# Performance work log

Hardware: AMD Instinct MI355X
Metric: run time of the kernel (lower is better)

Reference implementation:

```python
import jax, jax.numpy as jnp
import numpy as np

LAMBDA_SOFTMAX = 9.0  # opt.lambda_softmax (smooth)
LAMBDA_LSE = 6.0      # opt.lambda_lse (LogSumExp aggregation)
EPS = 1e-8


def l2norm(x, axis, eps=EPS):
    # matches torch l2norm: x / (sqrt(sum(x^2)) + eps)
    return x / (jnp.sqrt(jnp.sum(x * x, axis=axis, keepdims=True)) + eps)


def setup_inputs() -> dict:
    key = jax.random.key(0)
    k1, k2 = jax.random.split(key)
    images = jax.random.normal(k1, (128, 36, 256), dtype=jnp.float32)    # (n_image, n_regions, d)
    captions = jax.random.normal(k2, (256, 48, 256), dtype=jnp.float32)  # (n_caption, max_n_word, d)
    return {"images": images, "captions": captions}


def reference(images, captions):
    """Vectorized SCAN xattn_score_t2i with raw_feature_norm='clipped_l2norm',
    agg_func='LogSumExp'. Returns (n_image, n_caption) similarity matrix.
    Axes: c=caption, i=image, r=region (sourceL), w=word (queryL), d=embed."""
    # func_attention: attn = bmm(context, query^T) -> (b, sourceL, queryL); here batched over (c, i)
    attn = jnp.einsum('ird,cwd->cirw', images, captions)       # [c,i,r,w]
    # first norm: LeakyReLU(0.1) then l2norm over queryL dim (torch dim=2 of (b,r,w))
    attn = jax.nn.leaky_relu(attn, negative_slope=0.1)
    attn = l2norm(attn, axis=3)
    # transpose to (b, queryL, sourceL) and smoothed softmax over sourceL
    attn = jnp.swapaxes(attn, 2, 3)                            # [c,i,w,r]
    attn = jax.nn.softmax(attn * LAMBDA_SOFTMAX, axis=-1)
    # weightedContext = attn @ context  -> (b, queryL, d)
    wctx = jnp.einsum('ciwr,ird->ciwd', attn, images)          # [c,i,w,d]
    # cosine similarity over d between expanded caption words and weighted context
    cap = captions[:, None, :, :]                              # [c,1,w,d]
    w12 = jnp.sum(cap * wctx, axis=-1)                         # [c,i,w]
    w1 = jnp.sqrt(jnp.sum(cap * cap, axis=-1))
    w2 = jnp.sqrt(jnp.sum(wctx * wctx, axis=-1))
    row_sim = w12 / jnp.maximum(w1 * w2, EPS)                  # [c,i,w]
    # LogSumExp aggregation over words: log(sum exp(s*lse)) / lse
    sim = jax.scipy.special.logsumexp(row_sim * LAMBDA_LSE, axis=-1) / LAMBDA_LSE  # [c,i]
    return sim.T                                               # (n_image, n_caption)
```

## Files before the change

### kernel.cpp

```cpp
#include <hip/hip_runtime.h>
#include <math.h>

#define NI 128
#define NC 256
#define NR 36
#define NW 48
#define ND 256

#define PIB 264
#define PG  72
#define PSP 52

#define SOFT_SCALE 12.984255368000671f
#define LSE_SCALE   8.656170245333781f

typedef __bf16 bf16;
typedef __bf16 bf16x8 __attribute__((ext_vector_type(8)));
typedef __bf16 bf16x4 __attribute__((ext_vector_type(4)));
typedef float  f32x4  __attribute__((ext_vector_type(4)));

#define OFF_IB    0
#define OFF_G     19008
#define OFF_P     24192
#define OFF_GUARD 37504
#define SMEM_TOTAL 37632

#define MFMA16(A,B,C) __builtin_amdgcn_mfma_f32_16x16x32_bf16(A, B, C, 0, 0, 0)

__device__ __forceinline__ float dpp_add16(float v) {
    int x = __builtin_bit_cast(int, v);
    v += __builtin_bit_cast(float, __builtin_amdgcn_update_dpp(0, x, 0xB1, 0xF, 0xF, true));
    x = __builtin_bit_cast(int, v);
    v += __builtin_bit_cast(float, __builtin_amdgcn_update_dpp(0, x, 0x4E, 0xF, 0xF, true));
    x = __builtin_bit_cast(int, v);
    v += __builtin_bit_cast(float, __builtin_amdgcn_update_dpp(0, x, 0x141, 0xF, 0xF, true));
    x = __builtin_bit_cast(int, v);
    v += __builtin_bit_cast(float, __builtin_amdgcn_update_dpp(0, x, 0x140, 0xF, 0xF, true));
    return v;
}

__device__ __forceinline__ float lrelu(float t) {
    return __builtin_fmaf(0.55f, t, 0.45f * __builtin_fabsf(t));
}

__global__ __launch_bounds__(256)
void prep_kernel(const float* __restrict__ captions, bf16* __restrict__ capb,
                 float* __restrict__ w1g)
{
    const int c = blockIdx.x >> 2, q = blockIdx.x & 3;
    const int wave = threadIdx.x >> 6, lane = threadIdx.x & 63;
    #pragma unroll
    for (int j = 0; j < 3; ++j) {
        int w = q * 12 + wave * 3 + j;
        size_t off = ((size_t)c * NW + w) * ND + lane * 4;
        float4 v = *(const float4*)(captions + off);
        bf16x4 h = { (bf16)v.x, (bf16)v.y, (bf16)v.z, (bf16)v.w };
        *(bf16x4*)(capb + off) = h;
        float s = v.x*v.x + v.y*v.y + v.z*v.z + v.w*v.w;
        s += __shfl_xor(s, 1);  s += __shfl_xor(s, 2);  s += __shfl_xor(s, 4);
        s += __shfl_xor(s, 8);  s += __shfl_xor(s, 16); s += __shfl_xor(s, 32);
        if (lane == 0) w1g[c * NW + w] = LSE_SCALE / sqrtf(s);
    }
}

__device__ __forceinline__ bf16x8 ld_cvt_f32(const float* p, float& ss) {
    float4 lo = *(const float4*)p;
    float4 hi = *(const float4*)(p + 4);
    ss += lo.x*lo.x + lo.y*lo.y + lo.z*lo.z + lo.w*lo.w
        + hi.x*hi.x + hi.y*hi.y + hi.z*hi.z + hi.w*hi.w;
    bf16x8 r = { (bf16)lo.x, (bf16)lo.y, (bf16)lo.z, (bf16)lo.w,
                 (bf16)hi.x, (bf16)hi.y, (bf16)hi.z, (bf16)hi.w };
    return r;
}

#define STAGE_W(MT, BUF, W12) do {                                                      \
    _Pragma("unroll")                                                                   \
    for (int p = 0; p < 4; ++p) {                                                       \
        float a0v = acc[MT][0][p], a1v = acc[MT][1][p], a2v = acc[MT][2][p];            \
        float e0 = exp2f(__builtin_fmaf(c1[0], a0v, c2[0] * __builtin_fabsf(a0v)));     \
        float e1 = exp2f(__builtin_fmaf(c1[1], a1v, c2[1] * __builtin_fabsf(a1v)));     \
        float e2 = (l15 >= 12)                                                          \
            ? exp2f(__builtin_fmaf(c1[2], a2v, c2[2] * __builtin_fabsf(a2v)))           \
            : 0.f;                                                   \
        W12[p] = e0 * a0v + e1 * a1v + e2 * a2v;                                        \
        acc[MT][0][p] = e0; acc[MT][1][p] = e1; acc[MT][2][p] = e2;       \
        int row = quad * 4 + p;                                                         \
        (BUF)[row * PSP + l15]      = (bf16)e0;                                         \
        (BUF)[row * PSP + 16 + l15] = (bf16)e1;                                         \
        if (l15 >= 12) (BUF)[row * PSP + rb2 + l15] = (bf16)e2;        \
    }                                                                                   \
} while (0)

#define STAGE_R(MT, BUF, W12) do {                                                      \
    const bf16* ap = (BUF) + l15 * PSP;                                                 \
    bf16x8 pa0 = *(const bf16x8*)(ap + quad * 8);                                       \
    bf16x8 pa1 = *(const bf16x8*)(ap + 32 + quad * 8);  \
    f32x4 pg0 = {0,0,0,0}, pg1 = {0,0,0,0}, pg2 = {0,0,0,0};                            \
    {                                                                                   \
        bf16x8 t0 = *(const bf16x8*)&sG[(l15) * PG + quad * 8];                         \
        bf16x8 t1 = *(const bf16x8*)&sG[(l15) * PG + 32 + quad * 8];                    \
        pg0 = MFMA16(pa0, t0, pg0); pg0 = MFMA16(pa1, t1, pg0);                         \
        bf16x8 t2 = *(const bf16x8*)&sG[(16 + l15) * PG + quad * 8];                    \
        bf16x8 t3 = *(const bf16x8*)&sG[(16 + l15) * PG + 32 + quad * 8];               \
        pg1 = MFMA16(pa0, t2, pg1); pg1 = MFMA16(pa1, t3, pg1);                         \
        bf16x8 t4 = *(const bf16x8*)&sG[(rb2 + l15) * PG + quad * 8];                   \
        bf16x8 t5 = *(const bf16x8*)&sG[(rb2 + l15) * PG + 32 + quad * 8];              \
        pg2 = MFMA16(pa0, t4, pg2); pg2 = MFMA16(pa1, t5, pg2);                         \
    }                                                                                   \
    float4 wq = {0.f, 0.f, 0.f, 0.f};                                                   \
    if constexpr (USE_WS)                                                               \
        wq = *(const float4*)&w1g[(size_t)c * NW + (MT) * 16 + quad * 4];               \
    _Pragma("unroll")                                                                   \
    for (int p = 0; p < 4; ++p) {                                                       \
        float s2 = pg0[p] * acc[MT][0][p] + pg1[p] * acc[MT][1][p]                      \
                 + pg2[p] * acc[MT][2][p];                       \
        s2 = dpp_add16(s2);                                                             \
        float w12 = dpp_add16(W12[p]);                                                  \
        float wf = USE_WS ? ((const float*)&wq)[p] : w1f[MT][p];                        \
        esum += exp2f(w12 * __frsqrt_rn(fmaxf(s2, 1e-16f)) * wf);                       \
    }                                                                                   \
} while (0)

template<bool USE_WS>
__global__ __attribute__((amdgpu_flat_work_group_size(256, 256), amdgpu_waves_per_eu(4, 8)))
void scan_main(const float* __restrict__ images,
               const float* __restrict__ captions,
               const bf16* __restrict__ capb,
               const float* __restrict__ w1g,
               float* __restrict__ out)
{
    __shared__ __align__(16) unsigned char smem[SMEM_TOTAL];
    bf16* sIb = (bf16*)(smem + OFF_IB);
    bf16* sG  = (bf16*)(smem + OFF_G);

    const int tid  = threadIdx.x;
    const int wave = tid >> 6;
    const int lane = tid & 63;
    const int quad = lane >> 4;
    const int l15  = lane & 15;
    const int i    = blockIdx.x >> 4;
    const int c0   = (blockIdx.x & 15) * 16;

    bf16* bufA = (bf16*)(smem + OFF_P) + wave * (32 * PSP);
    bf16* bufB = bufA + 16 * PSP;

    const int rb2 = 20;

    const float* gI = images + (size_t)i * NR * ND;
    #pragma unroll
    for (int k = 0; k < 9; ++k) {
        int t = tid + k * 256;
        int e = t * 4, r = e >> 8, d = e & 255;
        float4 v = *(const float4*)(gI + e);
        bf16x4 h = { (bf16)v.x, (bf16)v.y, (bf16)v.z, (bf16)v.w };
        *(bf16x4*)&sIb[r * PIB + d] = h;
    }
    {
        uint32_t* pG = (uint32_t*)sG;
        #pragma unroll
        for (int k = 0; k < 6; ++k) { int x = tid + k * 256; if (x < 1296) pG[x] = 0u; }
        uint32_t* pP = (uint32_t*)(smem + OFF_P);
        #pragma unroll
        for (int k = 0; k < 14; ++k) { int x = tid + k * 256; if (x < 3360) pP[x] = 0u; }
    }
    __syncthreads();

    if (wave < 3) {
        const int mb = (wave == 2) ? rb2 : wave * 16;
        f32x4 g0 = {0,0,0,0}, g1 = {0,0,0,0}, g2 = {0,0,0,0};
        #pragma unroll
        for (int ks = 0; ks < 8; ++ks) {
            bf16x8 a  = *(const bf16x8*)&sIb[(mb + l15)  * PIB + ks * 32 + quad * 8];
            bf16x8 b0 = *(const bf16x8*)&sIb[(l15)       * PIB + ks * 32 + quad * 8];
            bf16x8 b1 = *(const bf16x8*)&sIb[(16 + l15)  * PIB + ks * 32 + quad * 8];
            bf16x8 b2 = *(const bf16x8*)&sIb[(rb2 + l15) * PIB + ks * 32 + quad * 8];
            g0 = MFMA16(a, b0, g0); g1 = MFMA16(a, b1, g1); g2 = MFMA16(a, b2, g2);
        }
        #pragma unroll
        for (int p = 0; p < 4; ++p) {
            int m = mb + quad * 4 + p;
            sG[m * PG + l15]       = (bf16)g0[p];
            sG[m * PG + 16 + l15]  = (bf16)g1[p];
            sG[m * PG + rb2 + l15] = (bf16)g2[p];
        }
    }
    __syncthreads();

    for (int it = 0; it < 4; ++it) {
        const int c = c0 + wave * 4 + it;

        f32x4 acc[3][3] = {};
        float ssc[3] = {0.f, 0.f, 0.f};
        float w1f[3][4] = {};
        const bf16*  ab   = USE_WS ? capb + ((size_t)c * NW + l15) * ND + quad * 8 : nullptr;
        const float* ab32 = USE_WS ? nullptr : captions + ((size_t)c * NW + l15) * ND + quad * 8;
        #pragma unroll
        for (int ks = 0; ks < 8; ++ks) {
            bf16x8 a0, a1, a2;
            if (USE_WS) {
                a0 = *(const bf16x8*)(ab + ks * 32);
                a1 = *(const bf16x8*)(ab + 16 * ND + ks * 32);
                a2 = *(const bf16x8*)(ab + 32 * ND + ks * 32);
            } else {
                a0 = ld_cvt_f32(ab32 + ks * 32, ssc[0]);
                a1 = ld_cvt_f32(ab32 + 16 * ND + ks * 32, ssc[1]);
                a2 = ld_cvt_f32(ab32 + 32 * ND + ks * 32, ssc[2]);
            }
            bf16x8 b0 = *(const bf16x8*)&sIb[(l15)       * PIB + ks * 32 + quad * 8];
            bf16x8 b1 = *(const bf16x8*)&sIb[(16 + l15)  * PIB + ks * 32 + quad * 8];
            bf16x8 b2 = *(const bf16x8*)&sIb[(rb2 + l15) * PIB + ks * 32 + quad * 8];
            acc[0][0] = MFMA16(a0, b0, acc[0][0]);
            acc[1][0] = MFMA16(a1, b0, acc[1][0]);
            acc[2][0] = MFMA16(a2, b0, acc[2][0]);
            acc[0][1] = MFMA16(a0, b1, acc[0][1]);
            acc[1][1] = MFMA16(a1, b1, acc[1][1]);
            acc[2][1] = MFMA16(a2, b1, acc[2][1]);
            acc[0][2] = MFMA16(a0, b2, acc[0][2]);
            acc[1][2] = MFMA16(a1, b2, acc[1][2]);
            acc[2][2] = MFMA16(a2, b2, acc[2][2]);
        }
        if (!USE_WS) {
            #pragma unroll
            for (int mt = 0; mt < 3; ++mt) {
                float s = ssc[mt];
                s += __shfl_xor(s, 16); s += __shfl_xor(s, 32);
                ssc[mt] = LSE_SCALE * __frsqrt_rn(fmaxf(s, 1e-16f));
            }
            #pragma unroll
            for (int mt = 0; mt < 3; ++mt)
                #pragma unroll
                for (int p = 0; p < 4; ++p)
                    w1f[mt][p] = __shfl(ssc[mt], (lane & 48) + quad * 4 + p);
        }

        float c1[3], c2[3];
        #pragma unroll
        for (int nt = 0; nt < 3; ++nt) {
            float s = 0.f;
            #pragma unroll
            for (int mt = 0; mt < 3; ++mt)
                #pragma unroll
                for (int p = 0; p < 4; ++p) { float t = lrelu(acc[mt][nt][p]); s += t * t; }
            s += __shfl_xor(s, 16); s += __shfl_xor(s, 32);
            float inv = SOFT_SCALE * __frsqrt_rn(fmaxf(s, 1e-12f));
            c1[nt] = 0.55f * inv;
            c2[nt] = 0.45f * inv;
        }

        float esum = 0.f;
        float w12a[4], w12b[4], w12c[4];
        STAGE_W(0, bufA, w12a);
        STAGE_W(1, bufB, w12b);
        STAGE_R(0, bufA, w12a);
        STAGE_W(2, bufA, w12c);
        STAGE_R(1, bufB, w12b);
        STAGE_R(2, bufA, w12c);

        esum += __shfl_xor(esum, 16); esum += __shfl_xor(esum, 32);
        if (lane == 0) out[(size_t)i * NC + c] = logf(esum) * (1.0f / 6.0f);
    }
}

extern "C" void kernel_launch(void* const* d_in, const int* in_sizes, int n_in,
                              void* d_out, int out_size, void* d_ws, size_t ws_size,
                              hipStream_t stream) {
    const float* images   = (const float*)d_in[0];
    const float* captions = (const float*)d_in[1];
    float* out = (float*)d_out;

    const size_t need_w1  = (size_t)NC * NW * sizeof(float);
    const size_t need_cap = (size_t)NC * NW * ND * 2;
    bool use_ws = ws_size >= need_w1 + need_cap;

    dim3 grid(2048), block(256);
    if (use_ws) {
        float* w1g = (float*)d_ws;
        bf16*  capb = (bf16*)((char*)d_ws + need_w1);
        hipLaunchKernelGGL(prep_kernel, dim3(1024), dim3(256), 0, stream, captions, capb, w1g);
        hipLaunchKernelGGL((scan_main<true>), grid, block, 0, stream, images, captions, capb, w1g, out);
    } else {
        hipLaunchKernelGGL((scan_main<false>), grid, block, 0, stream, images, captions,
                           (const bf16*)nullptr, (const float*)nullptr, out);
    }
}
```

Before: 164.6 us.

## Software-pipeline next caption's QK MFMAs under current caption's softmax epilogue

In the workspace path, the per-wave caption loop is unrolled with two accumulator sets. The QK^T MFMA steps for the next caption are interleaved between the exp/LDS/second-MFMA stages of the current caption. This is meant to hide global-load latency and overlap MFMA with the VALU/transcendental epilogue. It doubles accumulator register use, so the occupancy hint is lowered from 4 to 3 waves per EU, which risks less latency hiding across waves.

```diff
diff --git a/kernel.cpp b/kernel.cpp
--- a/kernel.cpp
+++ b/kernel.cpp
@@ -73,17 +73,17 @@
     return r;
 }
 
-#define STAGE_W(MT, BUF, W12) do {                                                      \
+#define STAGE_W(ACC, MT, BUF, W12) do {                                                 \
     _Pragma("unroll")                                                                   \
     for (int p = 0; p < 4; ++p) {                                                       \
-        float a0v = acc[MT][0][p], a1v = acc[MT][1][p], a2v = acc[MT][2][p];            \
+        float a0v = ACC[MT][0][p], a1v = ACC[MT][1][p], a2v = ACC[MT][2][p];            \
         float e0 = exp2f(__builtin_fmaf(c1[0], a0v, c2[0] * __builtin_fabsf(a0v)));     \
         float e1 = exp2f(__builtin_fmaf(c1[1], a1v, c2[1] * __builtin_fabsf(a1v)));     \
         float e2 = (l15 >= 12)                                                          \
             ? exp2f(__builtin_fmaf(c1[2], a2v, c2[2] * __builtin_fabsf(a2v)))           \
             : 0.f;                                                   \
         W12[p] = e0 * a0v + e1 * a1v + e2 * a2v;                                        \
-        acc[MT][0][p] = e0; acc[MT][1][p] = e1; acc[MT][2][p] = e2;       \
+        ACC[MT][0][p] = e0; ACC[MT][1][p] = e1; ACC[MT][2][p] = e2;       \
         int row = quad * 4 + p;                                                         \
         (BUF)[row * PSP + l15]      = (bf16)e0;                                         \
         (BUF)[row * PSP + 16 + l15] = (bf16)e1;                                         \
@@ -91,7 +91,7 @@
     }                                                                                   \
 } while (0)
 
-#define STAGE_R(MT, BUF, W12) do {                                                      \
+#define STAGE_R(ACC, MT, BUF, W12) do {                                                 \
     const bf16* ap = (BUF) + l15 * PSP;                                                 \
     bf16x8 pa0 = *(const bf16x8*)(ap + quad * 8);                                       \
     bf16x8 pa1 = *(const bf16x8*)(ap + 32 + quad * 8);  \
@@ -112,8 +112,8 @@
         wq = *(const float4*)&w1g[(size_t)c * NW + (MT) * 16 + quad * 4];               \
     _Pragma("unroll")                                                                   \
     for (int p = 0; p < 4; ++p) {                                                       \
-        float s2 = pg0[p] * acc[MT][0][p] + pg1[p] * acc[MT][1][p]                      \
-                 + pg2[p] * acc[MT][2][p];                       \
+        float s2 = pg0[p] * ACC[MT][0][p] + pg1[p] * ACC[MT][1][p]                      \
+                 + pg2[p] * ACC[MT][2][p];                       \
         s2 = dpp_add16(s2);                                                             \
         float w12 = dpp_add16(W12[p]);                                                  \
         float wf = USE_WS ? ((const float*)&wq)[p] : w1f[MT][p];                        \
@@ -122,7 +122,7 @@
 } while (0)
 
 template<bool USE_WS>
-__global__ __attribute__((amdgpu_flat_work_group_size(256, 256), amdgpu_waves_per_eu(4, 8)))
+__global__ __attribute__((amdgpu_flat_work_group_size(256, 256), amdgpu_waves_per_eu(3, 8)))
 void scan_main(const float* __restrict__ images,
                const float* __restrict__ captions,
                const bf16* __restrict__ capb,
@@ -186,40 +186,102 @@
     }
     __syncthreads();
 
-    for (int it = 0; it < 4; ++it) {
-        const int c = c0 + wave * 4 + it;
-
-        f32x4 acc[3][3] = {};
-        float ssc[3] = {0.f, 0.f, 0.f};
+    if constexpr (USE_WS) {
+        const size_t cstep = (size_t)NW * ND;
+        const bf16* ab0 = capb + ((size_t)(c0 + wave * 4) * NW + l15) * ND + quad * 8;
         float w1f[3][4] = {};
-        const bf16*  ab   = USE_WS ? capb + ((size_t)c * NW + l15) * ND + quad * 8 : nullptr;
-        const float* ab32 = USE_WS ? nullptr : captions + ((size_t)c * NW + l15) * ND + quad * 8;
-        #pragma unroll
-        for (int ks = 0; ks < 8; ++ks) {
-            bf16x8 a0, a1, a2;
-            if (USE_WS) {
-                a0 = *(const bf16x8*)(ab + ks * 32);
-                a1 = *(const bf16x8*)(ab + 16 * ND + ks * 32);
-                a2 = *(const bf16x8*)(ab + 32 * ND + ks * 32);
-            } else {
-                a0 = ld_cvt_f32(ab32 + ks * 32, ssc[0]);
-                a1 = ld_cvt_f32(ab32 + 16 * ND + ks * 32, ssc[1]);
-                a2 = ld_cvt_f32(ab32 + 32 * ND + ks * 32, ssc[2]);
-            }
+
+        auto qk_step = [&](f32x4 (&A)[3][3], const bf16* ab, int ks) {
+            bf16x8 a0 = *(const bf16x8*)(ab + ks * 32);
+            bf16x8 a1 = *(const bf16x8*)(ab + 16 * ND + ks * 32);
+            bf16x8 a2 = *(const bf16x8*)(ab + 32 * ND + ks * 32);
             bf16x8 b0 = *(const bf16x8*)&sIb[(l15)       * PIB + ks * 32 + quad * 8];
             bf16x8 b1 = *(const bf16x8*)&sIb[(16 + l15)  * PIB + ks * 32 + quad * 8];
             bf16x8 b2 = *(const bf16x8*)&sIb[(rb2 + l15) * PIB + ks * 32 + quad * 8];
-            acc[0][0] = MFMA16(a0, b0, acc[0][0]);
-            acc[1][0] = MFMA16(a1, b0, acc[1][0]);
-            acc[2][0] = MFMA16(a2, b0, acc[2][0]);
-            acc[0][1] = MFMA16(a0, b1, acc[0][1]);
-            acc[1][1] = MFMA16(a1, b1, acc[1][1]);
-            acc[2][1] = MFMA16(a2, b1, acc[2][1]);
-            acc[0][2] = MFMA16(a0, b2, acc[0][2]);
-            acc[1][2] = MFMA16(a1, b2, acc[1][2]);
-            acc[2][2] = MFMA16(a2, b2, acc[2][2]);
+            A[0][0] = MFMA16(a0, b0, A[0][0]);
+            A[1][0] = MFMA16(a1, b0, A[1][0]);
+            A[2][0] = MFMA16(a2, b0, A[2][0]);
+            A[0][1] = MFMA16(a0, b1, A[0][1]);
+            A[1][1] = MFMA16(a1, b1, A[1][1]);
+            A[2][1] = MFMA16(a2, b1, A[2][1]);
+            A[0][2] = MFMA16(a0, b2, A[0][2]);
+            A[1][2] = MFMA16(a1, b2, A[1][2]);
+            A[2][2] = MFMA16(a2, b2, A[2][2]);
+        };
+
+        f32x4 accP[3][3] = {}, accQ[3][3];
+        #pragma unroll
+        for (int ks = 0; ks < 8; ++ks) qk_step(accP, ab0, ks);
+
+        #pragma unroll
+        for (int it = 0; it < 4; ++it) {
+            f32x4 (&cur)[3][3] = (it & 1) ? accQ : accP;
+            f32x4 (&nxt)[3][3] = (it & 1) ? accP : accQ;
+            const bf16* abn = ab0 + (size_t)(it + 1) * cstep;
+            const int c = c0 + wave * 4 + it;
+
+            if (it < 3) {
+                #pragma unroll
+                for (int x = 0; x < 3; ++x)
+                    #pragma unroll
+                    for (int y = 0; y < 3; ++y) nxt[x][y] = (f32x4){0.f, 0.f, 0.f, 0.f};
+            }
+
+            float c1[3], c2[3];
+            #pragma unroll
+            for (int nt = 0; nt < 3; ++nt) {
+                float s = 0.f;
+                #pragma unroll
+                for (int mt = 0; mt < 3; ++mt)
+                    #pragma unroll
+                    for (int p = 0; p < 4; ++p) { float t = lrelu(cur[mt][nt][p]); s += t * t; }
+                s += __shfl_xor(s, 16); s += __shfl_xor(s, 32);
+                float inv = SOFT_SCALE * __frsqrt_rn(fmaxf(s, 1e-12f));
+                c1[nt] = 0.55f * inv;
+                c2[nt] = 0.45f * inv;
+            }
+            if (it < 3) { qk_step(nxt, abn, 0); qk_step(nxt, abn, 1); }
+
+            float esum = 0.f;
+            float w12a[4], w12b[4], w12c[4];
+            STAGE_W(cur, 0, bufA, w12a);
+            STAGE_W(cur, 1, bufB, w12b);
+            STAGE_R(cur, 0, bufA, w12a);
+            if (it < 3) { qk_step(nxt, abn, 2); qk_step(nxt, abn, 3); }
+            STAGE_W(cur, 2, bufA, w12c);
+            STAGE_R(cur, 1, bufB, w12b);
+            if (it < 3) { qk_step(nxt, abn, 4); qk_step(nxt, abn, 5); }
+            STAGE_R(cur, 2, bufA, w12c);
+            if (it < 3) { qk_step(nxt, abn, 6); qk_step(nxt, abn, 7); }
+
+            esum += __shfl_xor(esum, 16); esum += __shfl_xor(esum, 32);
+            if (lane == 0) out[(size_t)i * NC + c] = logf(esum) * (1.0f / 6.0f);
         }
-        if (!USE_WS) {
+    } else {
+        for (int it = 0; it < 4; ++it) {
+            const int c = c0 + wave * 4 + it;
+            f32x4 acc[3][3] = {};
+            float ssc[3] = {0.f, 0.f, 0.f};
+            float w1f[3][4] = {};
+            const float* ab32 = captions + ((size_t)c * NW + l15) * ND + quad * 8;
+            #pragma unroll
+            for (int ks = 0; ks < 8; ++ks) {
+                bf16x8 a0 = ld_cvt_f32(ab32 + ks * 32, ssc[0]);
+                bf16x8 a1 = ld_cvt_f32(ab32 + 16 * ND + ks * 32, ssc[1]);
+                bf16x8 a2 = ld_cvt_f32(ab32 + 32 * ND + ks * 32, ssc[2]);
+                bf16x8 b0 = *(const bf16x8*)&sIb[(l15)       * PIB + ks * 32 + quad * 8];
+                bf16x8 b1 = *(const bf16x8*)&sIb[(16 + l15)  * PIB + ks * 32 + quad * 8];
+                bf16x8 b2 = *(const bf16x8*)&sIb[(rb2 + l15) * PIB + ks * 32 + quad * 8];
+                acc[0][0] = MFMA16(a0, b0, acc[0][0]);
+                acc[1][0] = MFMA16(a1, b0, acc[1][0]);
+                acc[2][0] = MFMA16(a2, b0, acc[2][0]);
+                acc[0][1] = MFMA16(a0, b1, acc[0][1]);
+                acc[1][1] = MFMA16(a1, b1, acc[1][1]);
+                acc[2][1] = MFMA16(a2, b1, acc[2][1]);
+                acc[0][2] = MFMA16(a0, b2, acc[0][2]);
+                acc[1][2] = MFMA16(a1, b2, acc[1][2]);
+                acc[2][2] = MFMA16(a2, b2, acc[2][2]);
+            }
             #pragma unroll
             for (int mt = 0; mt < 3; ++mt) {
                 float s = ssc[mt];
@@ -231,33 +293,32 @@
                 #pragma unroll
                 for (int p = 0; p < 4; ++p)
                     w1f[mt][p] = __shfl(ssc[mt], (lane & 48) + quad * 4 + p);
+
+            float c1[3], c2[3];
+            #pragma unroll
+            for (int nt = 0; nt < 3; ++nt) {
+                float s = 0.f;
+                #pragma unroll
+                for (int mt = 0; mt < 3; ++mt)
+                    #pragma unroll
+                    for (int p = 0; p < 4; ++p) { float t = lrelu(acc[mt][nt][p]); s += t * t; }
+                s += __shfl_xor(s, 16); s += __shfl_xor(s, 32);
+                float inv = SOFT_SCALE * __frsqrt_rn(fmaxf(s, 1e-12f));
+                c1[nt] = 0.55f * inv; c2[nt] = 0.45f * inv;
+            }
+
+            float esum = 0.f;
+            float w12a[4], w12b[4], w12c[4];
+            STAGE_W(acc, 0, bufA, w12a);
+            STAGE_W(acc, 1, bufB, w12b);
+            STAGE_R(acc, 0, bufA, w12a);
+            STAGE_W(acc, 2, bufA, w12c);
+            STAGE_R(acc, 1, bufB, w12b);
+            STAGE_R(acc, 2, bufA, w12c);
+
+            esum += __shfl_xor(esum, 16); esum += __shfl_xor(esum, 32);
+            if (lane == 0) out[(size_t)i * NC + c] = logf(esum) * (1.0f / 6.0f);
         }
-
-        float c1[3], c2[3];
-        #pragma unroll
-        for (int nt = 0; nt < 3; ++nt) {
-            float s = 0.f;
-            #pragma unroll
-            for (int mt = 0; mt < 3; ++mt)
-                #pragma unroll
-                for (int p = 0; p < 4; ++p) { float t = lrelu(acc[mt][nt][p]); s += t * t; }
-            s += __shfl_xor(s, 16); s += __shfl_xor(s, 32);
-            float inv = SOFT_SCALE * __frsqrt_rn(fmaxf(s, 1e-12f));
-            c1[nt] = 0.55f * inv;
-            c2[nt] = 0.45f * inv;
-        }
-
-        float esum = 0.f;
-        float w12a[4], w12b[4], w12c[4];
-        STAGE_W(0, bufA, w12a);
-        STAGE_W(1, bufB, w12b);
-        STAGE_R(0, bufA, w12a);
-        STAGE_W(2, bufA, w12c);
-        STAGE_R(1, bufB, w12b);
-        STAGE_R(2, bufA, w12c);
-
-        esum += __shfl_xor(esum, 16); esum += __shfl_xor(esum, 32);
-        if (lane == 0) out[(size_t)i * NC + c] = logf(esum) * (1.0f / 6.0f);
     }
 }
 
```

New measurement: 174.4 us. 6.0% more time.
